# Kernel optimization log

Hardware: AMD Instinct MI355X
Metric: run time of the kernel (lower is better)

Reference implementation:

```python
import jax, jax.numpy as jnp
import numpy as np

DIM = 128
B, N = 4, 4096


def setup_inputs() -> dict:
    key = jax.random.key(0)
    k1, k2, k3 = jax.random.split(key, 3)
    return {
        "key": jax.random.normal(k1, (B, N, DIM), dtype=jnp.float32),
        "query": jax.random.normal(k2, (B, N, DIM), dtype=jnp.float32),
        "value": jax.random.normal(k3, (B, N, DIM), dtype=jnp.float32),
    }


def reference(key, query, value):
    # score[b, i, j] = <query[b, i], key[b, j]> / sqrt(dim)
    inv_sqrt_dim = 1.0 / jnp.sqrt(jnp.float32(DIM))
    score = jnp.einsum("bqd,bkd->bqk", query, key) * inv_sqrt_dim
    attn = jax.nn.softmax(score, axis=-1)
    context = jnp.einsum("bqk,bkd->bqd", attn, value)
    return (context, attn)
```

## Files before the change

### kernel.cpp

```cpp
#include <hip/hip_runtime.h>
#include <hip/hip_bf16.h>

#define BDIM 4
#define NSEQ 4096
#define DHEAD 128
#define SCALE 0.08838834764831845f

typedef __bf16 bf16x8 __attribute__((ext_vector_type(8)));
typedef float f32x4 __attribute__((ext_vector_type(4)));
typedef float f32x16 __attribute__((ext_vector_type(16)));
typedef unsigned int u32x4 __attribute__((ext_vector_type(4)));

__device__ __forceinline__ unsigned short f2bf(float f){
    return __builtin_bit_cast(unsigned short, (__bf16)f);
}
__device__ __forceinline__ unsigned long long pack4(float4 u){
    return (unsigned long long)f2bf(u.x)
         | ((unsigned long long)f2bf(u.y) << 16)
         | ((unsigned long long)f2bf(u.z) << 32)
         | ((unsigned long long)f2bf(u.w) << 48);
}
__device__ __forceinline__ void gload_lds16(const void* g, void* l){
    __builtin_amdgcn_global_load_lds(
        (const __attribute__((address_space(1))) unsigned int*)g,
        (__attribute__((address_space(3))) unsigned int*)l, 16, 0, 0);
}

extern "C" __global__ __launch_bounds__(256, 4)
void attn_stats(const float* __restrict__ K, const float* __restrict__ Q,
                float* __restrict__ pbase, int pstride)
{
    __shared__ __align__(16) char Klds[64 * 256];

    const int bid = blockIdx.x;
    const int ks  = bid & 3;
    const int rt  = (bid >> 2) & 63;
    const int b   = bid >> 8;
    const int tid = threadIdx.x;
    const int lane = tid & 63;
    const int w    = tid >> 6;
    const int g    = lane >> 4;
    const int c    = lane & 15;
    const int rowbase = rt * 64;

    const float* qrow = Q + ((size_t)b * NSEQ + rowbase + w * 16 + c) * DHEAD;
    bf16x8 qf[4];
#pragma unroll
    for (int kk = 0; kk < 4; kk++) {
        const float4* p0 = (const float4*)(qrow + g * 8 + kk * 32);
        float4 u = p0[0], v = p0[1];
        bf16x8 t;
        t[0] = (__bf16)(u.x * SCALE); t[1] = (__bf16)(u.y * SCALE);
        t[2] = (__bf16)(u.z * SCALE); t[3] = (__bf16)(u.w * SCALE);
        t[4] = (__bf16)(v.x * SCALE); t[5] = (__bf16)(v.y * SCALE);
        t[6] = (__bf16)(v.z * SCALE); t[7] = (__bf16)(v.w * SCALE);
        qf[kk] = t;
    }

    float m[4], l[4];
#pragma unroll
    for (int r = 0; r < 4; r++) { m[r] = -1e30f; l[r] = 0.0f; }

    const int f  = tid & 31;
    const int r0 = tid >> 5;

    for (int kt = 0; kt < 16; kt++) {
        const float* ktile = K + ((size_t)b * NSEQ + ks * 1024 + kt * 64) * DHEAD;
#pragma unroll
        for (int i = 0; i < 8; i++) {
            int r = r0 + i * 8;
            float4 u = *(const float4*)(ktile + (size_t)r * DHEAD + f * 4);
            *(unsigned long long*)(Klds + r * 256 + ((f * 8) ^ ((r & 7) << 4))) = pack4(u);
        }
        __syncthreads();

        f32x4 acc[4];
#pragma unroll
        for (int n = 0; n < 4; n++) acc[n] = (f32x4){0.f, 0.f, 0.f, 0.f};
#pragma unroll
        for (int n = 0; n < 4; n++) {
            int row = n * 16 + c;
#pragma unroll
            for (int kk = 0; kk < 4; kk++) {
                bf16x8 kf = *(const bf16x8*)(Klds + row * 256 +
                                ((g * 16 + kk * 64) ^ ((row & 7) << 4)));
                acc[n] = __builtin_amdgcn_mfma_f32_16x16x32_bf16(qf[kk], kf, acc[n], 0, 0, 0);
            }
        }

#pragma unroll
        for (int r = 0; r < 4; r++) {
            float t = fmaxf(fmaxf(acc[0][r], acc[1][r]), fmaxf(acc[2][r], acc[3][r]));
            t = fmaxf(t, __shfl_xor(t, 1));
            t = fmaxf(t, __shfl_xor(t, 2));
            t = fmaxf(t, __shfl_xor(t, 4));
            t = fmaxf(t, __shfl_xor(t, 8));
            float mn = fmaxf(m[r], t);
            float sc = __expf(m[r] - mn);
            float ps = __expf(acc[0][r] - mn) + __expf(acc[1][r] - mn)
                     + __expf(acc[2][r] - mn) + __expf(acc[3][r] - mn);
            ps += __shfl_xor(ps, 1);
            ps += __shfl_xor(ps, 2);
            ps += __shfl_xor(ps, 4);
            ps += __shfl_xor(ps, 8);
            l[r] = l[r] * sc + ps;
            m[r] = mn;
        }
        __syncthreads();
    }

    if (c == 0) {
#pragma unroll
        for (int r = 0; r < 4; r++) {
            size_t row = rowbase + w * 16 + g * 4 + r;
            float* p = pbase + ((size_t)b * NSEQ + row) * pstride + ks * 2;
            p[0] = m[r];
            p[1] = l[r];
        }
    }
}

extern "C" __global__ __launch_bounds__(256, 4)
void repack3(const float* __restrict__ K, const float* __restrict__ V,
             char* __restrict__ ws)
{
    const int bid = blockIdx.x;
    const int T = bid & 127;
    const int b = bid >> 7;
    const int tid = threadIdx.x;

    char* Kp = ws + ((size_t)(b * 128 + T) << 14);
    const float* Ks = K + ((size_t)b * NSEQ + T * 32) * DHEAD;
    const float* Vs = V + ((size_t)b * NSEQ + T * 32) * DHEAD;

#pragma unroll
    for (int i = 0; i < 2; i++) {
        int u = tid + 256 * i;
        int ds = u >> 6, ln = u & 63;
        int m = ln & 31, hi = ln >> 5;
        const float* s = Ks + (size_t)m * DHEAD + ds * 16 + hi * 8;
        float4 a = *(const float4*)s;
        float4 bq = *(const float4*)(s + 4);
        ulonglong2 wv;
        wv.x = pack4(a);
        wv.y = pack4(bq);
        *(ulonglong2*)(Kp + u * 16) = wv;
    }
#pragma unroll
    for (int i = 0; i < 2; i++) {
        int u = tid + 256 * i;
        int f = u >> 6, ln = u & 63;
        int dg = f >> 1, kb = f & 1;
        int dd = ln & 31, hi = ln >> 5;
        int d = dg * 32 + dd;
        const float* s = Vs + (size_t)(kb * 16 + hi * 8) * DHEAD + d;
        float v0 = s[0 * DHEAD], v1 = s[1 * DHEAD], v2 = s[2 * DHEAD], v3 = s[3 * DHEAD];
        float v4 = s[4 * DHEAD], v5 = s[5 * DHEAD], v6 = s[6 * DHEAD], v7 = s[7 * DHEAD];
        ulonglong2 wv;
        wv.x = (unsigned long long)f2bf(v0)
             | ((unsigned long long)f2bf(v1) << 16)
             | ((unsigned long long)f2bf(v2) << 32)
             | ((unsigned long long)f2bf(v3) << 48);
        wv.y = (unsigned long long)f2bf(v4)
             | ((unsigned long long)f2bf(v5) << 16)
             | ((unsigned long long)f2bf(v6) << 32)
             | ((unsigned long long)f2bf(v7) << 48);
        *(ulonglong2*)(Kp + 8192 + u * 16) = wv;
    }
}

extern "C" __global__ __launch_bounds__(256, 3)
void attn_mf2(const char* __restrict__ ws, const float* __restrict__ Q,
              float* __restrict__ out, float* __restrict__ part, int use_atomic)
{
    __shared__ __align__(16) char LDS[32768];

    const int bid = blockIdx.x;
    const int ks  = bid & 7;
    const int qt  = (bid >> 3) & 31;
    const int b   = bid >> 8;
    const int tid = threadIdx.x;
    const int wv  = tid >> 6;
    const int lane = tid & 63;
    const int hi   = lane >> 5;
    const int qq   = lane & 31;
    const int q    = qt * 128 + wv * 32 + qq;

    float* attn = out + (size_t)BDIM * NSEQ * DHEAD;
    const float* pb = (const float*)(ws + (8u << 20));

    float Cq;
    {
        const float* prow = pb + ((size_t)b * NSEQ + q) * 8;
        float4 p0 = *(const float4*)prow;
        float4 p1 = *(const float4*)(prow + 4);
        float M = fmaxf(fmaxf(p0.x, p0.z), fmaxf(p1.x, p1.z));
        float L = p0.y * __expf(p0.x - M) + p0.w * __expf(p0.z - M)
                + p1.y * __expf(p1.x - M) + p1.w * __expf(p1.z - M);
        Cq = M + __logf(L);
    }

    const float* qrow = Q + ((size_t)b * NSEQ + q) * DHEAD;
    bf16x8 qf[8];
#pragma unroll
    for (int ds = 0; ds < 8; ds++) {
        const float4* p0 = (const float4*)(qrow + ds * 16 + hi * 8);
        float4 u = p0[0], v = p0[1];
        bf16x8 t;
        t[0] = (__bf16)(u.x * SCALE); t[1] = (__bf16)(u.y * SCALE);
        t[2] = (__bf16)(u.z * SCALE); t[3] = (__bf16)(u.w * SCALE);
        t[4] = (__bf16)(v.x * SCALE); t[5] = (__bf16)(v.y * SCALE);
        t[6] = (__bf16)(v.z * SCALE); t[7] = (__bf16)(v.w * SCALE);
        qf[ds] = t;
    }

    f32x16 ctx[4];
#pragma unroll
    for (int dg = 0; dg < 4; dg++) ctx[dg] = (f32x16)(0.0f);

    const char* img = ws + ((size_t)(b * 128 + ks * 16) << 14);

#pragma unroll
    for (int i = 0; i < 4; i++) {
        int o = tid * 16 + i * 4096;
        gload_lds16(img + o, LDS + o);
    }

    float* arowb = attn + ((size_t)b * NSEQ + q) * NSEQ + ks * 512 + 4 * hi;

    for (int kt = 0; kt < 16; kt++) {
        __builtin_amdgcn_s_barrier();
        __builtin_amdgcn_sched_barrier(0);
        if (kt < 15) {
            const char* src = img + ((size_t)(kt + 1) << 14);
            char* dst = LDS + (((kt + 1) & 1) << 14);
#pragma unroll
            for (int i = 0; i < 4; i++) {
                int o = tid * 16 + i * 4096;
                gload_lds16(src + o, dst + o);
            }
            asm volatile("s_waitcnt vmcnt(4)" ::: "memory");
        } else {
            asm volatile("s_waitcnt vmcnt(0)" ::: "memory");
        }
        __builtin_amdgcn_s_barrier();
        __builtin_amdgcn_sched_barrier(0);

        const char* bufc = LDS + ((kt & 1) << 14);

        f32x16 s0 = (f32x16)(0.0f), s1 = (f32x16)(0.0f);
        __builtin_amdgcn_s_setprio(1);
#pragma unroll
        for (int dp = 0; dp < 4; dp++) {
            bf16x8 kfa = *(const bf16x8*)(bufc + (2 * dp) * 1024 + lane * 16);
            bf16x8 kfb = *(const bf16x8*)(bufc + (2 * dp + 1) * 1024 + lane * 16);
            s0 = __builtin_amdgcn_mfma_f32_32x32x16_bf16(kfa, qf[2 * dp], s0, 0, 0, 0);
            s1 = __builtin_amdgcn_mfma_f32_32x32x16_bf16(kfb, qf[2 * dp + 1], s1, 0, 0, 0);
        }
        __builtin_amdgcn_s_setprio(0);

        float p[16];
#pragma unroll
        for (int r = 0; r < 16; r++) p[r] = __expf((s0[r] + s1[r]) - Cq);

        float* arow = arowb + kt * 32;
#pragma unroll
        for (int j = 0; j < 4; j++) {
            float4 pv = {p[4 * j], p[4 * j + 1], p[4 * j + 2], p[4 * j + 3]};
            *(float4*)(arow + 8 * j) = pv;
        }

        unsigned int bpk[8], sb[8];
#pragma unroll
        for (int i = 0; i < 8; i++)
            bpk[i] = (unsigned int)f2bf(p[2 * i]) | ((unsigned int)f2bf(p[2 * i + 1]) << 16);
#pragma unroll
        for (int i = 0; i < 8; i++)
            sb[i] = (unsigned int)__shfl_xor((int)bpk[i], 32);

        u32x4 w0, w1;
        w0[0] = hi ? sb[2] : bpk[0];
        w0[1] = hi ? sb[3] : bpk[1];
        w0[2] = hi ? bpk[2] : sb[0];
        w0[3] = hi ? bpk[3] : sb[1];
        w1[0] = hi ? sb[6] : bpk[4];
        w1[1] = hi ? sb[7] : bpk[5];
        w1[2] = hi ? bpk[6] : sb[4];
        w1[3] = hi ? bpk[7] : sb[5];
        bf16x8 pf0 = __builtin_bit_cast(bf16x8, w0);
        bf16x8 pf1 = __builtin_bit_cast(bf16x8, w1);

        __builtin_amdgcn_s_setprio(1);
#pragma unroll
        for (int dg = 0; dg < 4; dg++) {
            bf16x8 vf0 = *(const bf16x8*)(bufc + 8192 + (dg * 2 + 0) * 1024 + lane * 16);
            bf16x8 vf1 = *(const bf16x8*)(bufc + 8192 + (dg * 2 + 1) * 1024 + lane * 16);
            ctx[dg] = __builtin_amdgcn_mfma_f32_32x32x16_bf16(vf0, pf0, ctx[dg], 0, 0, 0);
            ctx[dg] = __builtin_amdgcn_mfma_f32_32x32x16_bf16(vf1, pf1, ctx[dg], 0, 0, 0);
        }
        __builtin_amdgcn_s_setprio(0);
    }

    if (!use_atomic) {
        float* cp = part + (((size_t)(ks * 4 + b) * NSEQ + q) * DHEAD) + 4 * hi;
#pragma unroll
        for (int dg = 0; dg < 4; dg++)
#pragma unroll
            for (int j = 0; j < 4; j++) {
                float4 v = {ctx[dg][4 * j], ctx[dg][4 * j + 1],
                            ctx[dg][4 * j + 2], ctx[dg][4 * j + 3]};
                *(float4*)(cp + dg * 32 + 8 * j) = v;
            }
    } else {
        float* cp = out + ((size_t)b * NSEQ + q) * DHEAD + 4 * hi;
#pragma unroll
        for (int dg = 0; dg < 4; dg++)
#pragma unroll
            for (int j = 0; j < 4; j++)
#pragma unroll
                for (int e = 0; e < 4; e++)
                    atomicAdd(cp + dg * 32 + 8 * j + e, ctx[dg][4 * j + e]);
    }
}

extern "C" __global__ __launch_bounds__(256, 4)
void ctx_reduce8(const float4* __restrict__ part, float4* __restrict__ out)
{
    const size_t gt = (size_t)blockIdx.x * 256 + threadIdx.x;
    const size_t stride = (size_t)BDIM * NSEQ * DHEAD / 4;
    float4 s = part[gt];
#pragma unroll
    for (int i = 1; i < 8; i++) {
        float4 a = part[gt + (size_t)i * stride];
        s.x += a.x; s.y += a.y; s.z += a.z; s.w += a.w;
    }
    out[gt] = s;
}

extern "C" __global__ __launch_bounds__(512, 2)
void attn_final_fb(const float* __restrict__ K, const float* __restrict__ Q,
                   const float* __restrict__ V, float* __restrict__ out)
{
    __shared__ __align__(16) char LDS[81920];

    const int bid = blockIdx.x;
    const int rt  = bid & 63;
    const int b   = bid >> 6;
    const int tid = threadIdx.x;
    const int rowbase = rt * 64;
    const int lane = tid & 63;
    const int w    = tid >> 6;
    const int rw   = w & 3;
    const int grp  = w >> 2;
    const int g    = lane >> 4;
    const int c    = lane & 15;
    const int t    = tid & 255;

    float* ctxOut = out;
    float* attn   = out + (size_t)BDIM * NSEQ * DHEAD;

    char* Klds  = LDS + grp * 16384;
    char* Vtlds = LDS + 32768 + grp * 16384;
    char* Plds  = LDS + 65536 + w * 2048;

    float Cq;
    {
        const float* prow = attn + ((size_t)b * NSEQ + rowbase + rw * 16 + c) * NSEQ;
        float4 p0 = *(const float4*)prow;
        float4 p1 = *(const float4*)(prow + 4);
        float M = fmaxf(fmaxf(p0.x, p0.z), fmaxf(p1.x, p1.z));
        float L = p0.y * __expf(p0.x - M) + p0.w * __expf(p0.z - M)
                + p1.y * __expf(p1.x - M) + p1.w * __expf(p1.z - M);
        Cq = M + __logf(L);
    }

    const float* qrow = Q + ((size_t)b * NSEQ + rowbase + rw * 16 + c) * DHEAD;
    bf16x8 qf[4];
#pragma unroll
    for (int kk = 0; kk < 4; kk++) {
        const float4* p0 = (const float4*)(qrow + g * 8 + kk * 32);
        float4 u = p0[0], v = p0[1];
        bf16x8 tt;
        tt[0] = (__bf16)(u.x * SCALE); tt[1] = (__bf16)(u.y * SCALE);
        tt[2] = (__bf16)(u.z * SCALE); tt[3] = (__bf16)(u.w * SCALE);
        tt[4] = (__bf16)(v.x * SCALE); tt[5] = (__bf16)(v.y * SCALE);
        tt[6] = (__bf16)(v.z * SCALE); tt[7] = (__bf16)(v.w * SCALE);
        qf[kk] = tt;
    }

    f32x4 ctx[8];
#pragma unroll
    for (int n2 = 0; n2 < 8; n2++) ctx[n2] = (f32x4){0.f, 0.f, 0.f, 0.f};

    __syncthreads();

    const int fK = t & 31;
    const int rK = t >> 5;
    const int dq = t & 15;
    const int kb = t >> 4;
    const int k0 = kb * 4;
    const int d0 = dq * 2;

    const float* kbase = K + ((size_t)b * NSEQ + grp * 2048) * DHEAD;
    const float* vbase = V + ((size_t)b * NSEQ + grp * 2048) * DHEAD;

    float4 kreg[8];
    float2 vreg[4][4];

#pragma unroll
    for (int i = 0; i < 8; i++)
        kreg[i] = *(const float4*)(kbase + (size_t)(rK + i * 8) * DHEAD + fK * 4);
#pragma unroll
    for (int i = 0; i < 4; i++)
#pragma unroll
        for (int j = 0; j < 4; j++)
            vreg[i][j] = *(const float2*)(vbase + (size_t)(k0 + j) * DHEAD + d0 + 32 * i);

    for (int kt = 0; kt < 32; kt++) {
        __builtin_amdgcn_s_barrier();

#pragma unroll
        for (int i = 0; i < 8; i++) {
            int row = rK + i * 8;
            *(unsigned long long*)(Klds + row * 256 + ((fK * 8) ^ ((row & 7) << 4))) = pack4(kreg[i]);
        }
#pragma unroll
        for (int i = 0; i < 4; i++) {
            int d = d0 + 32 * i;
            unsigned long long rr0 =
                (unsigned long long)f2bf(vreg[i][0].x)
              | ((unsigned long long)f2bf(vreg[i][1].x) << 16)
              | ((unsigned long long)f2bf(vreg[i][2].x) << 32)
              | ((unsigned long long)f2bf(vreg[i][3].x) << 48);
            unsigned long long rr1 =
                (unsigned long long)f2bf(vreg[i][0].y)
              | ((unsigned long long)f2bf(vreg[i][1].y) << 16)
              | ((unsigned long long)f2bf(vreg[i][2].y) << 32)
              | ((unsigned long long)f2bf(vreg[i][3].y) << 48);
            int swz = (d & 7) << 4;
            *(unsigned long long*)(Vtlds + d * 128 + ((k0 * 2) ^ swz)) = rr0;
            *(unsigned long long*)(Vtlds + (d + 1) * 128 + ((k0 * 2) ^ (swz + 16))) = rr1;
        }
        asm volatile("s_waitcnt lgkmcnt(0)" ::: "memory");
        __builtin_amdgcn_s_barrier();

        {
            int kn = (kt + 1) & 31;
            const float* kp = kbase + (size_t)kn * 64 * DHEAD;
            const float* vp = vbase + (size_t)kn * 64 * DHEAD;
#pragma unroll
            for (int i = 0; i < 8; i++)
                kreg[i] = *(const float4*)(kp + (size_t)(rK + i * 8) * DHEAD + fK * 4);
#pragma unroll
            for (int i = 0; i < 4; i++)
#pragma unroll
                for (int j = 0; j < 4; j++)
                    vreg[i][j] = *(const float2*)(vp + (size_t)(k0 + j) * DHEAD + d0 + 32 * i);
        }

        f32x4 sacc[4];
#pragma unroll
        for (int nt = 0; nt < 4; nt++) sacc[nt] = (f32x4){0.f, 0.f, 0.f, 0.f};
        __builtin_amdgcn_s_setprio(1);
#pragma unroll
        for (int nt = 0; nt < 4; nt++) {
            int row = nt * 16 + c;
#pragma unroll
            for (int kk = 0; kk < 4; kk++) {
                bf16x8 kf = *(const bf16x8*)(Klds + row * 256 +
                                ((g * 16 + kk * 64) ^ ((row & 7) << 4)));
                sacc[nt] = __builtin_amdgcn_mfma_f32_16x16x32_bf16(kf, qf[kk], sacc[nt], 0, 0, 0);
            }
        }
        __builtin_amdgcn_s_setprio(0);

        const int col0 = grp * 2048 + kt * 64;
        float* arow = attn + ((size_t)b * NSEQ + rowbase + rw * 16 + c) * NSEQ + col0;
#pragma unroll
        for (int nt = 0; nt < 4; nt++) {
            float4 pv;
            pv.x = __expf(sacc[nt][0] - Cq);
            pv.y = __expf(sacc[nt][1] - Cq);
            pv.z = __expf(sacc[nt][2] - Cq);
            pv.w = __expf(sacc[nt][3] - Cq);
            *(float4*)(arow + nt * 16 + g * 4) = pv;
            *(unsigned long long*)(Plds + c * 128 +
                ((nt * 32 + g * 8) ^ ((c & 7) << 4))) = pack4(pv);
        }
        asm volatile("s_waitcnt lgkmcnt(0)" ::: "memory");
        __builtin_amdgcn_sched_barrier(0);

        bf16x8 pf[2];
#pragma unroll
        for (int kk = 0; kk < 2; kk++)
            pf[kk] = *(const bf16x8*)(Plds + c * 128 +
                        ((kk * 64 + g * 16) ^ ((c & 7) << 4)));

        __builtin_amdgcn_s_setprio(1);
#pragma unroll
        for (int n2 = 0; n2 < 8; n2++) {
            int d = n2 * 16 + c;
#pragma unroll
            for (int kk = 0; kk < 2; kk++) {
                bf16x8 vff = *(const bf16x8*)(Vtlds + d * 128 +
                                ((kk * 64 + g * 16) ^ ((d & 7) << 4)));
                ctx[n2] = __builtin_amdgcn_mfma_f32_16x16x32_bf16(pf[kk], vff, ctx[n2], 0, 0, 0);
            }
        }
        __builtin_amdgcn_s_setprio(0);
    }

    __syncthreads();

    float* red = (float*)LDS;
    if (grp == 1) {
#pragma unroll
        for (int n2 = 0; n2 < 8; n2++)
#pragma unroll
            for (int r = 0; r < 4; r++)
                red[(rw * 16 + g * 4 + r) * 128 + n2 * 16 + c] = ctx[n2][r];
    }
    __syncthreads();
    if (grp == 0) {
#pragma unroll
        for (int n2 = 0; n2 < 8; n2++)
#pragma unroll
            for (int r = 0; r < 4; r++) {
                size_t row = rowbase + rw * 16 + g * 4 + r;
                ctxOut[((size_t)b * NSEQ + row) * DHEAD + n2 * 16 + c] =
                    ctx[n2][r] + red[(rw * 16 + g * 4 + r) * 128 + n2 * 16 + c];
            }
    }
}

extern "C" void kernel_launch(void* const* d_in, const int* in_sizes, int n_in,
                              void* d_out, int out_size, void* d_ws, size_t ws_size,
                              hipStream_t stream)
{
    const float* K = (const float*)d_in[0];
    const float* Q = (const float*)d_in[1];
    const float* V = (const float*)d_in[2];
    float* out  = (float*)d_out;
    float* attn = out + (size_t)BDIM * NSEQ * DHEAD;

    const size_t ctx_bytes  = (size_t)BDIM * NSEQ * DHEAD * sizeof(float);
    const size_t need_part  = (9u << 20) + 8 * ctx_bytes;
    const size_t need_atom  = (9u << 20);

    if (ws_size >= need_part) {
        char* ws = (char*)d_ws;
        float* pb = (float*)(ws + (8u << 20));
        float* part = (float*)(ws + (9u << 20));
        attn_stats<<<dim3(4 * 64 * 4), dim3(256), 0, stream>>>(K, Q, pb, 8);
        repack3<<<dim3(4 * 128), dim3(256), 0, stream>>>(K, V, ws);
        attn_mf2<<<dim3(1024), dim3(256), 0, stream>>>(ws, Q, out, part, 0);
        ctx_reduce8<<<dim3(2048), dim3(256), 0, stream>>>((const float4*)part, (float4*)out);
    } else if (ws_size >= need_atom) {
        char* ws = (char*)d_ws;
        float* pb = (float*)(ws + (8u << 20));
        hipMemsetAsync(out, 0, ctx_bytes, stream);
        attn_stats<<<dim3(4 * 64 * 4), dim3(256), 0, stream>>>(K, Q, pb, 8);
        repack3<<<dim3(4 * 128), dim3(256), 0, stream>>>(K, V, ws);
        attn_mf2<<<dim3(1024), dim3(256), 0, stream>>>(ws, Q, out, out, 1);
    } else {
        attn_stats<<<dim3(4 * 64 * 4), dim3(256), 0, stream>>>(K, Q, attn, NSEQ);
        attn_final_fb<<<dim3(4 * 64), dim3(512), 0, stream>>>(K, Q, V, out);
    }
}
```

Baseline: 162.7 us.

## Fuse stats and repack kernels, replace partial-sum reduction with atomics

The softmax-statistics kernel and the K/V bf16 repack kernel are merged into one launch, with extra blocks doing the repack. The path that wrote eight partial context buffers and reduced them in a separate kernel is dropped. The default path now zeroes the output with a memset and accumulates the split-K context directly with float atomicAdd. This removes two launches and the large partial-buffer write/read traffic, at the cost of atomic contention and nondeterministic summation order.

```diff
diff --git a/kernel.cpp b/kernel.cpp
--- a/kernel.cpp
+++ b/kernel.cpp
@@ -27,16 +27,65 @@
 }
 
 extern "C" __global__ __launch_bounds__(256, 4)
-void attn_stats(const float* __restrict__ K, const float* __restrict__ Q,
-                float* __restrict__ pbase, int pstride)
+void stats_repack(const float* __restrict__ K, const float* __restrict__ Q,
+                  const float* __restrict__ V, char* __restrict__ ws)
 {
+    const int bid0 = blockIdx.x;
+    const int tid = threadIdx.x;
+
+    if (bid0 >= 1024) {
+        const int rid = bid0 - 1024;
+        const int T = rid & 127;
+        const int b = rid >> 7;
+
+        char* Kp = ws + ((size_t)(b * 128 + T) << 14);
+        const float* Ks = K + ((size_t)b * NSEQ + T * 32) * DHEAD;
+        const float* Vs = V + ((size_t)b * NSEQ + T * 32) * DHEAD;
+
+#pragma unroll
+        for (int i = 0; i < 2; i++) {
+            int u = tid + 256 * i;
+            int ds = u >> 6, ln = u & 63;
+            int m = ln & 31, hi = ln >> 5;
+            const float* s = Ks + (size_t)m * DHEAD + ds * 16 + hi * 8;
+            float4 a = *(const float4*)s;
+            float4 bq = *(const float4*)(s + 4);
+            ulonglong2 wv;
+            wv.x = pack4(a);
+            wv.y = pack4(bq);
+            *(ulonglong2*)(Kp + u * 16) = wv;
+        }
+#pragma unroll
+        for (int i = 0; i < 2; i++) {
+            int u = tid + 256 * i;
+            int f = u >> 6, ln = u & 63;
+            int dg = f >> 1, kb = f & 1;
+            int dd = ln & 31, hi = ln >> 5;
+            int d = dg * 32 + dd;
+            const float* s = Vs + (size_t)(kb * 16 + hi * 8) * DHEAD + d;
+            float v0 = s[0 * DHEAD], v1 = s[1 * DHEAD], v2 = s[2 * DHEAD], v3 = s[3 * DHEAD];
+            float v4 = s[4 * DHEAD], v5 = s[5 * DHEAD], v6 = s[6 * DHEAD], v7 = s[7 * DHEAD];
+            ulonglong2 wv;
+            wv.x = (unsigned long long)f2bf(v0)
+                 | ((unsigned long long)f2bf(v1) << 16)
+                 | ((unsigned long long)f2bf(v2) << 32)
+                 | ((unsigned long long)f2bf(v3) << 48);
+            wv.y = (unsigned long long)f2bf(v4)
+                 | ((unsigned long long)f2bf(v5) << 16)
+                 | ((unsigned long long)f2bf(v6) << 32)
+                 | ((unsigned long long)f2bf(v7) << 48);
+            *(ulonglong2*)(Kp + 8192 + u * 16) = wv;
+        }
+        return;
+    }
+
     __shared__ __align__(16) char Klds[64 * 256];
 
-    const int bid = blockIdx.x;
+    float* pbase = (float*)(ws + (8u << 20));
+    const int bid = bid0;
     const int ks  = bid & 3;
     const int rt  = (bid >> 2) & 63;
     const int b   = bid >> 8;
-    const int tid = threadIdx.x;
     const int lane = tid & 63;
     const int w    = tid >> 6;
     const int g    = lane >> 4;
@@ -113,65 +162,16 @@
 #pragma unroll
         for (int r = 0; r < 4; r++) {
             size_t row = rowbase + w * 16 + g * 4 + r;
-            float* p = pbase + ((size_t)b * NSEQ + row) * pstride + ks * 2;
+            float* p = pbase + ((size_t)b * NSEQ + row) * 8 + ks * 2;
             p[0] = m[r];
             p[1] = l[r];
         }
     }
 }
 
-extern "C" __global__ __launch_bounds__(256, 4)
-void repack3(const float* __restrict__ K, const float* __restrict__ V,
-             char* __restrict__ ws)
-{
-    const int bid = blockIdx.x;
-    const int T = bid & 127;
-    const int b = bid >> 7;
-    const int tid = threadIdx.x;
-
-    char* Kp = ws + ((size_t)(b * 128 + T) << 14);
-    const float* Ks = K + ((size_t)b * NSEQ + T * 32) * DHEAD;
-    const float* Vs = V + ((size_t)b * NSEQ + T * 32) * DHEAD;
-
-#pragma unroll
-    for (int i = 0; i < 2; i++) {
-        int u = tid + 256 * i;
-        int ds = u >> 6, ln = u & 63;
-        int m = ln & 31, hi = ln >> 5;
-        const float* s = Ks + (size_t)m * DHEAD + ds * 16 + hi * 8;
-        float4 a = *(const float4*)s;
-        float4 bq = *(const float4*)(s + 4);
-        ulonglong2 wv;
-        wv.x = pack4(a);
-        wv.y = pack4(bq);
-        *(ulonglong2*)(Kp + u * 16) = wv;
-    }
-#pragma unroll
-    for (int i = 0; i < 2; i++) {
-        int u = tid + 256 * i;
-        int f = u >> 6, ln = u & 63;
-        int dg = f >> 1, kb = f & 1;
-        int dd = ln & 31, hi = ln >> 5;
-        int d = dg * 32 + dd;
-        const float* s = Vs + (size_t)(kb * 16 + hi * 8) * DHEAD + d;
-        float v0 = s[0 * DHEAD], v1 = s[1 * DHEAD], v2 = s[2 * DHEAD], v3 = s[3 * DHEAD];
-        float v4 = s[4 * DHEAD], v5 = s[5 * DHEAD], v6 = s[6 * DHEAD], v7 = s[7 * DHEAD];
-        ulonglong2 wv;
-        wv.x = (unsigned long long)f2bf(v0)
-             | ((unsigned long long)f2bf(v1) << 16)
-             | ((unsigned long long)f2bf(v2) << 32)
-             | ((unsigned long long)f2bf(v3) << 48);
-        wv.y = (unsigned long long)f2bf(v4)
-             | ((unsigned long long)f2bf(v5) << 16)
-             | ((unsigned long long)f2bf(v6) << 32)
-             | ((unsigned long long)f2bf(v7) << 48);
-        *(ulonglong2*)(Kp + 8192 + u * 16) = wv;
-    }
-}
-
 extern "C" __global__ __launch_bounds__(256, 3)
 void attn_mf2(const char* __restrict__ ws, const float* __restrict__ Q,
-              float* __restrict__ out, float* __restrict__ part, int use_atomic)
+              float* __restrict__ out)
 {
     __shared__ __align__(16) char LDS[32768];
 
@@ -301,40 +301,108 @@
         __builtin_amdgcn_s_setprio(0);
     }
 
-    if (!use_atomic) {
-        float* cp = part + (((size_t)(ks * 4 + b) * NSEQ + q) * DHEAD) + 4 * hi;
-#pragma unroll
-        for (int dg = 0; dg < 4; dg++)
-#pragma unroll
-            for (int j = 0; j < 4; j++) {
-                float4 v = {ctx[dg][4 * j], ctx[dg][4 * j + 1],
-                            ctx[dg][4 * j + 2], ctx[dg][4 * j + 3]};
-                *(float4*)(cp + dg * 32 + 8 * j) = v;
+    float* cp = out + ((size_t)b * NSEQ + q) * DHEAD + 4 * hi;
+#pragma unroll
+    for (int dg = 0; dg < 4; dg++)
+#pragma unroll
+        for (int j = 0; j < 4; j++)
+#pragma unroll
+            for (int e = 0; e < 4; e++)
+                atomicAdd(cp + dg * 32 + 8 * j + e, ctx[dg][4 * j + e]);
+}
+
+extern "C" __global__ __launch_bounds__(256, 4)
+void attn_stats_fb(const float* __restrict__ K, const float* __restrict__ Q,
+                   float* __restrict__ pbase, int pstride)
+{
+    __shared__ __align__(16) char Klds[64 * 256];
+
+    const int bid = blockIdx.x;
+    const int ks  = bid & 3;
+    const int rt  = (bid >> 2) & 63;
+    const int b   = bid >> 8;
+    const int tid = threadIdx.x;
+    const int lane = tid & 63;
+    const int w    = tid >> 6;
+    const int g    = lane >> 4;
+    const int c    = lane & 15;
+    const int rowbase = rt * 64;
+
+    const float* qrow = Q + ((size_t)b * NSEQ + rowbase + w * 16 + c) * DHEAD;
+    bf16x8 qf[4];
+#pragma unroll
+    for (int kk = 0; kk < 4; kk++) {
+        const float4* p0 = (const float4*)(qrow + g * 8 + kk * 32);
+        float4 u = p0[0], v = p0[1];
+        bf16x8 t;
+        t[0] = (__bf16)(u.x * SCALE); t[1] = (__bf16)(u.y * SCALE);
+        t[2] = (__bf16)(u.z * SCALE); t[3] = (__bf16)(u.w * SCALE);
+        t[4] = (__bf16)(v.x * SCALE); t[5] = (__bf16)(v.y * SCALE);
+        t[6] = (__bf16)(v.z * SCALE); t[7] = (__bf16)(v.w * SCALE);
+        qf[kk] = t;
+    }
+
+    float m[4], l[4];
+#pragma unroll
+    for (int r = 0; r < 4; r++) { m[r] = -1e30f; l[r] = 0.0f; }
+
+    const int f  = tid & 31;
+    const int r0 = tid >> 5;
+
+    for (int kt = 0; kt < 16; kt++) {
+        const float* ktile = K + ((size_t)b * NSEQ + ks * 1024 + kt * 64) * DHEAD;
+#pragma unroll
+        for (int i = 0; i < 8; i++) {
+            int r = r0 + i * 8;
+            float4 u = *(const float4*)(ktile + (size_t)r * DHEAD + f * 4);
+            *(unsigned long long*)(Klds + r * 256 + ((f * 8) ^ ((r & 7) << 4))) = pack4(u);
+        }
+        __syncthreads();
+
+        f32x4 acc[4];
+#pragma unroll
+        for (int n = 0; n < 4; n++) acc[n] = (f32x4){0.f, 0.f, 0.f, 0.f};
+#pragma unroll
+        for (int n = 0; n < 4; n++) {
+            int row = n * 16 + c;
+#pragma unroll
+            for (int kk = 0; kk < 4; kk++) {
+                bf16x8 kf = *(const bf16x8*)(Klds + row * 256 +
+                                ((g * 16 + kk * 64) ^ ((row & 7) << 4)));
+                acc[n] = __builtin_amdgcn_mfma_f32_16x16x32_bf16(qf[kk], kf, acc[n], 0, 0, 0);
             }
-    } else {
-        float* cp = out + ((size_t)b * NSEQ + q) * DHEAD + 4 * hi;
-#pragma unroll
-        for (int dg = 0; dg < 4; dg++)
-#pragma unroll
-            for (int j = 0; j < 4; j++)
-#pragma unroll
-                for (int e = 0; e < 4; e++)
-                    atomicAdd(cp + dg * 32 + 8 * j + e, ctx[dg][4 * j + e]);
-    }
-}
-
-extern "C" __global__ __launch_bounds__(256, 4)
-void ctx_reduce8(const float4* __restrict__ part, float4* __restrict__ out)
-{
-    const size_t gt = (size_t)blockIdx.x * 256 + threadIdx.x;
-    const size_t stride = (size_t)BDIM * NSEQ * DHEAD / 4;
-    float4 s = part[gt];
-#pragma unroll
-    for (int i = 1; i < 8; i++) {
-        float4 a = part[gt + (size_t)i * stride];
-        s.x += a.x; s.y += a.y; s.z += a.z; s.w += a.w;
-    }
-    out[gt] = s;
+        }
+
+#pragma unroll
+        for (int r = 0; r < 4; r++) {
+            float t = fmaxf(fmaxf(acc[0][r], acc[1][r]), fmaxf(acc[2][r], acc[3][r]));
+            t = fmaxf(t, __shfl_xor(t, 1));
+            t = fmaxf(t, __shfl_xor(t, 2));
+            t = fmaxf(t, __shfl_xor(t, 4));
+            t = fmaxf(t, __shfl_xor(t, 8));
+            float mn = fmaxf(m[r], t);
+            float sc = __expf(m[r] - mn);
+            float ps = __expf(acc[0][r] - mn) + __expf(acc[1][r] - mn)
+                     + __expf(acc[2][r] - mn) + __expf(acc[3][r] - mn);
+            ps += __shfl_xor(ps, 1);
+            ps += __shfl_xor(ps, 2);
+            ps += __shfl_xor(ps, 4);
+            ps += __shfl_xor(ps, 8);
+            l[r] = l[r] * sc + ps;
+            m[r] = mn;
+        }
+        __syncthreads();
+    }
+
+    if (c == 0) {
+#pragma unroll
+        for (int r = 0; r < 4; r++) {
+            size_t row = rowbase + w * 16 + g * 4 + r;
+            float* p = pbase + ((size_t)b * NSEQ + row) * pstride + ks * 2;
+            p[0] = m[r];
+            p[1] = l[r];
+        }
+    }
 }
 
 extern "C" __global__ __launch_bounds__(512, 2)
@@ -543,27 +611,16 @@
     float* out  = (float*)d_out;
     float* attn = out + (size_t)BDIM * NSEQ * DHEAD;
 
-    const size_t ctx_bytes  = (size_t)BDIM * NSEQ * DHEAD * sizeof(float);
-    const size_t need_part  = (9u << 20) + 8 * ctx_bytes;
-    const size_t need_atom  = (9u << 20);
-
-    if (ws_size >= need_part) {
+    const size_t ctx_bytes = (size_t)BDIM * NSEQ * DHEAD * sizeof(float);
+    const size_t need      = (9u << 20);
+
+    if (ws_size >= need) {
         char* ws = (char*)d_ws;
-        float* pb = (float*)(ws + (8u << 20));
-        float* part = (float*)(ws + (9u << 20));
-        attn_stats<<<dim3(4 * 64 * 4), dim3(256), 0, stream>>>(K, Q, pb, 8);
-        repack3<<<dim3(4 * 128), dim3(256), 0, stream>>>(K, V, ws);
-        attn_mf2<<<dim3(1024), dim3(256), 0, stream>>>(ws, Q, out, part, 0);
-        ctx_reduce8<<<dim3(2048), dim3(256), 0, stream>>>((const float4*)part, (float4*)out);
-    } else if (ws_size >= need_atom) {
-        char* ws = (char*)d_ws;
-        float* pb = (float*)(ws + (8u << 20));
         hipMemsetAsync(out, 0, ctx_bytes, stream);
-        attn_stats<<<dim3(4 * 64 * 4), dim3(256), 0, stream>>>(K, Q, pb, 8);
-        repack3<<<dim3(4 * 128), dim3(256), 0, stream>>>(K, V, ws);
-        attn_mf2<<<dim3(1024), dim3(256), 0, stream>>>(ws, Q, out, out, 1);
+        stats_repack<<<dim3(1024 + 512), dim3(256), 0, stream>>>(K, Q, V, ws);
+        attn_mf2<<<dim3(1024), dim3(256), 0, stream>>>(ws, Q, out);
     } else {
-        attn_stats<<<dim3(4 * 64 * 4), dim3(256), 0, stream>>>(K, Q, attn, NSEQ);
+        attn_stats_fb<<<dim3(4 * 64 * 4), dim3(256), 0, stream>>>(K, Q, attn, NSEQ);
         attn_final_fb<<<dim3(4 * 64), dim3(512), 0, stream>>>(K, Q, V, out);
     }
 }
```

New measurement: 515.6 us. 3.17x slower.
